# Kernel optimization log

Measured on AMD Instinct MI355X. Metric: run time of the kernel, lower is better.

Reference implementation:

```python
import jax, jax.numpy as jnp
import numpy as np

# nqsystems=8 grouped sites, physical dim d=2^ncontraq=16,
# state bond r=64, layer (unitary MPO) bond rl=16, operator MPO bond ro=4,
# nlsystems=1 pre-contracted circuit layer.
NQ, R, D, RL, RO, NL = 8, 64, 16, 16, 4, 1


def setup_inputs() -> dict:
    key = jax.random.key(0)
    k1, k2, k3 = jax.random.split(key, 3)
    # scale so contractions stay O(1) numerically
    state = jax.random.normal(k1, (NQ, R, D, R), jnp.float32) / np.float32(np.sqrt(R * D))
    layer = jax.random.normal(k2, (NL, NQ, RL, D, D, RL), jnp.float32) / np.float32(np.sqrt(RL * D))
    operator = jax.random.normal(k3, (NQ, RO, D, D, RO), jnp.float32) / np.float32(np.sqrt(RO * D))
    return {"state": state, "layer": layer, "operator": operator}


def reference(state, layer, operator):
    """<psi| U^dagger O U |psi> contracted site-by-site along the TT chain.

    state:    [nq, r, d, r]        TT cores of |psi>
    layer:    [nl, nq, rl, d, d, rl]  TT-operator cores of the circuit layer (nl=1)
    operator: [nq, ro, d, d, ro]   TT-operator cores of the observable
    """
    r, rl, ro = state.shape[1], layer.shape[3], operator.shape[1]
    # open-boundary closure: boundary vectors = e0 on every bond
    env0 = jnp.zeros((r, rl, ro, rl, r), state.dtype).at[0, 0, 0, 0, 0].set(1.0)
    U = layer[0]  # nlsystems == 1

    def step(env, cores):
        S, Uq, Oq = cores
        # tt_dagger: conj + transpose physical indices (0,2,1,3)
        Ud = jnp.conj(Uq).transpose(0, 2, 1, 3)
        # env axes: a=bra-state bond, l=bra-layer bond, o=operator bond,
        #           m=ket-layer bond, b=ket-state bond
        t = jnp.einsum('alomb,aiA->lombiA', env, jnp.conj(S))   # bra state core
        t = jnp.einsum('lombiA,lijL->ombAjL', t, Ud)            # U^dagger core
        t = jnp.einsum('ombAjL,ojkO->mbALkO', t, Oq)            # observable core
        t = jnp.einsum('mbALkO,mksM->bALOsM', t, Uq)            # U core
        t = jnp.einsum('bALOsM,bsB->ALOMB', t, S)               # ket state core
        return t, None

    env, _ = jax.lax.scan(step, env0, (state, U, operator))
    return env[0, 0, 0, 0, 0]
```

## Files before the change

### kernel.cpp

```cpp
#include <hip/hip_runtime.h>


typedef __attribute__((ext_vector_type(8))) short bf16x8;
typedef __attribute__((ext_vector_type(8))) _Float16 f16x8;
typedef __attribute__((ext_vector_type(4))) float f32x4;
typedef __attribute__((ext_vector_type(4))) unsigned short us4;

static __device__ __forceinline__ unsigned short f2bf(float x) {
    union { float f; unsigned u; } a; a.f = x;
    return (unsigned short)((a.u + 0x7FFF + ((a.u >> 16) & 1)) >> 16);
}
static __device__ __forceinline__ float bf2f(unsigned short h) {
    union { unsigned u; float f; } a; a.u = (unsigned)h << 16; return a.f;
}
static __device__ __forceinline__ unsigned split2(float x) {
    unsigned short h = f2bf(x);
    unsigned short l = f2bf(x - bf2f(h));
    return (unsigned)h | ((unsigned)l << 16);
}
static __device__ __forceinline__ void split2_pair(float x0, float x1,
                                                   unsigned& o0, unsigned& o1) {
    unsigned hh, ll;
    asm("v_cvt_pk_bf16_f32 %0, %1, %2" : "=v"(hh) : "v"(x0), "v"(x1));
    union { unsigned u; float f; } c0, c1;
    c0.u = hh << 16;
    c1.u = hh & 0xffff0000u;
    float r0 = x0 - c0.f, r1 = x1 - c1.f;
    asm("v_cvt_pk_bf16_f32 %0, %1, %2" : "=v"(ll) : "v"(r0), "v"(r1));
    asm("v_perm_b32 %0, %1, %2, %3" : "=v"(o0) : "v"(ll), "v"(hh), "s"(0x05040100));
    asm("v_perm_b32 %0, %1, %2, %3" : "=v"(o1) : "v"(ll), "v"(hh), "s"(0x07060302));
}
static __device__ __forceinline__ unsigned short f2h_bits(float x) {
    union { _Float16 h; unsigned short u; } c; c.h = (_Float16)x; return c.u;
}
static __device__ __forceinline__ float h2f_bits(unsigned short u) {
    union { unsigned short u; _Float16 h; } c; c.u = u; return (float)c.h;
}
static __device__ __forceinline__ void gl_lds16(const unsigned short* g,
                                                unsigned short* l) {
    __builtin_amdgcn_global_load_lds(
        (const __attribute__((address_space(1))) unsigned int*)g,
        (__attribute__((address_space(3))) unsigned int*)l, 16, 0, 0);
}

__global__ void write_diag_kernel(float* out, float v) {
    if (threadIdx.x == 0 && blockIdx.x == 0) out[0] = v;
}
__global__ void zero_out(float* o) {
    if (threadIdx.x == 0 && blockIdx.x == 0) o[0] = 0.0f;
}

__global__ void prep_apack(const float* __restrict__ layer,
                           unsigned short* __restrict__ Ap2,
                           unsigned short* __restrict__ Ap4) {
    int idx = blockIdx.x * 256 + threadIdx.x;
    int q = idx >> 13, k0 = (idx >> 10) & 7, mt = (idx >> 6) & 15, lane = idx & 63;
    int quad = lane >> 4, r = lane & 15;
    unsigned short h2[8], l2[8], h4[8], l4[8];
#pragma unroll
    for (int j = 0; j < 8; j++) {
        int k = k0 * 32 + quad * 8 + j;
        int m = mt * 16 + r;
        float v2 = layer[(size_t)q * 65536 +
                         (size_t)((((k >> 4) * 16 + (m >> 4)) * 16 + (k & 15)) * 16 + (m & 15))];
        float v4 = layer[(size_t)q * 65536 +
                         (size_t)((((k >> 4) * 16 + (k & 15)) * 16 + (m >> 4)) * 16 + (m & 15))];
        h2[j] = f2h_bits(v2); l2[j] = f2h_bits(v2 - h2f_bits(h2[j]));
        h4[j] = f2h_bits(v4); l4[j] = f2h_bits(v4 - h2f_bits(h4[j]));
    }
    size_t base = ((size_t)((q * 8 + k0) * 16 + mt) * 2) * 512 + lane * 8;
    *(us4*)(Ap2 + base)       = *(us4*)&h2[0];
    *(us4*)(Ap2 + base + 4)   = *(us4*)&h2[4];
    *(us4*)(Ap2 + base + 512) = *(us4*)&l2[0];
    *(us4*)(Ap2 + base + 516) = *(us4*)&l2[4];
    *(us4*)(Ap4 + base)       = *(us4*)&h4[0];
    *(us4*)(Ap4 + base + 4)   = *(us4*)&h4[4];
    *(us4*)(Ap4 + base + 512) = *(us4*)&l4[0];
    *(us4*)(Ap4 + base + 516) = *(us4*)&l4[4];
}

__global__ void prep_spack1(const float* __restrict__ state,
                            unsigned short* __restrict__ Sp1) {
    int idx = blockIdx.x * 256 + threadIdx.x;
    int q = idx >> 13, c = (idx >> 11) & 3, k0 = (idx >> 10) & 1,
        mt = (idx >> 6) & 15, lane = idx & 63;
    int quad = lane >> 4, lr = lane & 15;
    unsigned short h[8], l[8];
#pragma unroll
    for (int j = 0; j < 8; j++) {
        int k = k0 * 32 + quad * 8 + j;
        float v = state[(size_t)q * 65536 + (size_t)(k * 16 + mt) * 64 + c * 16 + lr];
        h[j] = f2bf(v); l[j] = f2bf(v - bf2f(h[j]));
    }
    size_t base = (size_t)(q * 4 + c) * 32768 + ((size_t)(k0 * 16 + mt) * 2) * 512 + lane * 8;
    *(us4*)(Sp1 + base)       = *(us4*)&h[0];
    *(us4*)(Sp1 + base + 4)   = *(us4*)&h[4];
    *(us4*)(Sp1 + base + 512) = *(us4*)&l[0];
    *(us4*)(Sp1 + base + 516) = *(us4*)&l[4];
}

__global__ void prep_spack5(const float* __restrict__ state,
                            unsigned short* __restrict__ Sp5) {
    int idx = blockIdx.x * 256 + threadIdx.x;
    int q = idx >> 13, k0 = (idx >> 8) & 31, mt = (idx >> 6) & 3, lane = idx & 63;
    int quad = lane >> 4, lr = lane & 15;
    unsigned short h[8], l[8];
#pragma unroll
    for (int j = 0; j < 8; j++) {
        int k = k0 * 32 + quad * 8 + j;
        int s = k >> 6, b = k & 63;
        float v = state[(size_t)q * 65536 + (size_t)(b * 16 + s) * 64 + mt * 16 + lr];
        h[j] = f2bf(v); l[j] = f2bf(v - bf2f(h[j]));
    }
    size_t base = (size_t)q * 131072 + ((size_t)(k0 * 4 + mt) * 2) * 512 + lane * 8;
    *(us4*)(Sp5 + base)       = *(us4*)&h[0];
    *(us4*)(Sp5 + base + 4)   = *(us4*)&h[4];
    *(us4*)(Sp5 + base + 512) = *(us4*)&l[0];
    *(us4*)(Sp5 + base + 516) = *(us4*)&l[4];
}

__global__ void prep_opack3(const float* __restrict__ oper,
                            unsigned short* __restrict__ Op3) {
    int idx = blockIdx.x * 256 + threadIdx.x;
    int q = idx >> 9, k0 = (idx >> 8) & 1, mt = (idx >> 6) & 3, lane = idx & 63;
    int quad = lane >> 4, lr = lane & 15;
    unsigned short h[8], l[8];
#pragma unroll
    for (int j = 0; j < 8; j++) {
        int k = k0 * 32 + quad * 8 + j;
        int m = mt * 16 + lr;
        float v = oper[(size_t)q * 4096 + (size_t)(k * 16 + (m & 15)) * 4 + (m >> 4)];
        h[j] = f2h_bits(v); l[j] = f2h_bits(v - h2f_bits(h[j]));
    }
    size_t base = (size_t)q * 8192 + ((size_t)(k0 * 4 + mt) * 2) * 512 + lane * 8;
    *(us4*)(Op3 + base)       = *(us4*)&h[0];
    *(us4*)(Op3 + base + 4)   = *(us4*)&h[4];
    *(us4*)(Op3 + base + 512) = *(us4*)&l[0];
    *(us4*)(Op3 + base + 516) = *(us4*)&l[4];
}

__global__ void env_split_k(const float* __restrict__ env, unsigned* __restrict__ envS) {
    int t = blockIdx.x * 256 + threadIdx.x;
    float4 v = ((const float4*)env)[t];
    uint4 o;
    o.x = split2(v.x); o.y = split2(v.y); o.z = split2(v.z); o.w = split2(v.w);
    ((uint4*)envS)[t] = o;
}

__global__ void s0_g2(const float* __restrict__ state, const float* __restrict__ layer,
                      float* __restrict__ g2) {
    int t = blockIdx.x * 256 + threadIdx.x;
    int A = t >> 8, j = (t >> 4) & 15, L = t & 15;
    float s = 0;
    for (int i = 0; i < 16; i++) s += state[i * 64 + A] * layer[(j * 16 + i) * 16 + L];
    g2[t] = s;
}
__global__ void s0_g3(const float* __restrict__ g2, const float* __restrict__ oper,
                      float* __restrict__ g3) {
    int t = blockIdx.x * 256 + threadIdx.x;
    int A = t >> 10, L = (t >> 6) & 15, k = (t >> 2) & 15, O = t & 3;
    float s = 0;
    for (int j = 0; j < 16; j++) s += g2[A * 256 + j * 16 + L] * oper[(j * 16 + k) * 4 + O];
    g3[t] = s;
}
__global__ void s0_g4(const float* __restrict__ g3, const float* __restrict__ layer,
                      float* __restrict__ g4) {
    int t = blockIdx.x * 256 + threadIdx.x;
    int A = t >> 14, L = (t >> 10) & 15, O = (t >> 8) & 3, sp = (t >> 4) & 15, M = t & 15;
    float s = 0;
    for (int k = 0; k < 16; k++)
        s += g3[A * 1024 + L * 64 + k * 4 + O] * layer[(k * 16 + sp) * 16 + M];
    g4[t] = s;
}
__global__ void s0_env(const float* __restrict__ g4, const float* __restrict__ state,
                       float* __restrict__ env) {
    int t = blockIdx.x * 256 + threadIdx.x;
    int A = t >> 16, L = (t >> 12) & 15, O = (t >> 10) & 3, M = (t >> 6) & 15, B = t & 63;
    float s = 0;
    for (int sp = 0; sp < 16; sp++)
        s += g4[A * 16384 + L * 1024 + O * 256 + sp * 16 + M] * state[sp * 64 + B];
    env[(size_t)(L * 64 + O * 16 + M) * 4096 + A * 64 + B] = s;
}

__global__ void s7_c1(const float* __restrict__ state, const float* __restrict__ layer,
                      float* __restrict__ c1) {
    int t = blockIdx.x * 256 + threadIdx.x;
    int l = t >> 10, a = (t >> 4) & 63, j = t & 15;
    float s = 0;
    for (int i = 0; i < 16; i++)
        s += state[7 * 65536 + (a * 16 + i) * 64] * layer[7 * 65536 + ((l * 16 + j) * 16 + i) * 16];
    c1[t] = s;
}
__global__ void s7_c2(const float* __restrict__ c1, const float* __restrict__ oper,
                      float* __restrict__ c2) {
    int t = blockIdx.x * 256 + threadIdx.x;
    int o = t >> 14, l = (t >> 10) & 15, a = (t >> 4) & 63, k = t & 15;
    float s = 0;
    for (int j = 0; j < 16; j++)
        s += c1[l * 1024 + a * 16 + j] * oper[7 * 4096 + ((o * 16 + j) * 16 + k) * 4];
    c2[t] = s;
}
__global__ void s7_c3(const float* __restrict__ c2, const float* __restrict__ layer,
                      float* __restrict__ c3) {
    int t = blockIdx.x * 256 + threadIdx.x;
    int m = t >> 16, o = (t >> 14) & 3, l = (t >> 10) & 15, a = (t >> 4) & 63, sp = t & 15;
    float s = 0;
    for (int k = 0; k < 16; k++)
        s += c2[o * 16384 + l * 1024 + a * 16 + k] *
             layer[7 * 65536 + ((m * 16 + k) * 16 + sp) * 16];
    c3[t] = s;
}
__global__ void prep_sv(const float* __restrict__ state, float* __restrict__ sv) {
    int t = blockIdx.x * 256 + threadIdx.x;
    sv[t] = state[7 * 65536 + t * 64];
}
__global__ __launch_bounds__(256) void s7_fused(const float* __restrict__ env,
                                                const float* __restrict__ c3,
                                                const float* __restrict__ sv,
                                                float* __restrict__ out) {
    __shared__ float c3s[1024], svs[1024], red[256];
    int t = threadIdx.x;
    int n0 = blockIdx.x * 64;
    int l = n0 >> 12, o = (n0 >> 10) & 3, m = (n0 >> 6) & 15;
    const float* c3b = c3 + m * 65536 + o * 16384 + l * 1024;
    const float* eb  = env + (size_t)blockIdx.x * 4096;
    for (int i = t; i < 1024; i += 256) { c3s[i] = c3b[i]; svs[i] = sv[i]; }
    __syncthreads();
    float s = 0;
    int b = t & 63, ag = t >> 6;
#pragma unroll
    for (int g = 0; g < 16; g++) {
        int a = ag * 16 + g;
        float e = eb[a * 64 + b];
        float w = 0;
#pragma unroll
        for (int sp = 0; sp < 16; sp++) w += c3s[a * 16 + sp] * svs[b * 16 + sp];
        s += e * w;
    }
    red[t] = s; __syncthreads();
    for (int off = 128; off; off >>= 1) { if (t < off) red[t] += red[t + off]; __syncthreads(); }
    if (t == 0) atomicAdd(out, red[0]);
}

static __device__ __forceinline__ void g1_body(int bid, void* smem,
                                               const unsigned* __restrict__ envS,
                                               const unsigned short* __restrict__ Sp1,
                                               unsigned short* __restrict__ t1,
                                               float scale) {
    unsigned* Bt = (unsigned*)smem;
    const int tid = threadIdx.x, lane = tid & 63, wave = tid >> 6;
    const int quad = lane >> 4, lr = lane & 15;
    const int cc = bid >> 10, rid = bid & 1023;
    const int l = rid >> 6, o = (rid >> 4) & 3, m2 = rid & 15;

    f32x4 acc[4][4];
#pragma unroll
    for (int i = 0; i < 4; i++)
#pragma unroll
        for (int j = 0; j < 4; j++)
#pragma unroll
            for (int r = 0; r < 4; r++) acc[i][j][r] = 0.0f;

    const unsigned* Bv = envS + (size_t)rid * 4096;
    const unsigned short* Sp1c = Sp1 + (size_t)cc * 32768;
    uint4 ur[2];
    auto load_tile = [&](int k0) {
        const uint4* src = (const uint4*)(Bv + k0 * 2048);
        ur[0] = src[tid];
        ur[1] = src[256 + tid];
    };
    auto store_tile = [&]() {
#pragma unroll
        for (int v = 0; v < 2; v++) {
            int e = v * 256 + tid;
            unsigned* p = &Bt[(e >> 4) * 65 + (e & 15) * 4];
            p[0] = ur[v].x; p[1] = ur[v].y; p[2] = ur[v].z; p[3] = ur[v].w;
        }
    };

    bf16x8 ahb[2][4], alb[2][4];
    auto loadA = [&](int k0, int buf) {
#pragma unroll
        for (int mt = 0; mt < 4; mt++) {
            int gmt = wave * 4 + mt;
            const unsigned short* ap = Sp1c + ((size_t)(k0 * 16 + gmt) * 2) * 512 + lane * 8;
            ahb[buf][mt] = *(const bf16x8*)ap;
            alb[buf][mt] = *(const bf16x8*)(ap + 512);
        }
    };

    load_tile(0);
    loadA(0, 0);
    store_tile();
#pragma unroll
    for (int k0 = 0; k0 < 2; k0++) {
        __syncthreads();
        if (k0 + 1 < 2) { load_tile(k0 + 1); loadA(k0 + 1, 1); }
#pragma unroll
        for (int nt = 0; nt < 4; nt++) {
            int nl = nt * 16 + lr;
            bf16x8 bh, bl;
#pragma unroll
            for (int j = 0; j < 8; j++) {
                unsigned u = Bt[(quad * 8 + j) * 65 + nl];
                bh[j] = (short)(u & 0xffffu);
                bl[j] = (short)(u >> 16);
            }
#pragma unroll
            for (int mt = 0; mt < 4; mt++) {
                acc[mt][nt] = __builtin_amdgcn_mfma_f32_16x16x32_bf16(ahb[k0][mt], bh, acc[mt][nt], 0, 0, 0);
                acc[mt][nt] = __builtin_amdgcn_mfma_f32_16x16x32_bf16(ahb[k0][mt], bl, acc[mt][nt], 0, 0, 0);
                acc[mt][nt] = __builtin_amdgcn_mfma_f32_16x16x32_bf16(alb[k0][mt], bh, acc[mt][nt], 0, 0, 0);
            }
        }
        __syncthreads();
        if (k0 + 1 < 2) store_tile();
    }

#pragma unroll
    for (int nt = 0; nt < 4; nt++) {
        int b = nt * 16 + lr;
#pragma unroll
        for (int r = 0; r < 4; r++) {
            int a4 = quad * 4 + r;
            us4 w;
#pragma unroll
            for (int mt = 0; mt < 4; mt++) w[mt] = f2h_bits(acc[mt][nt][r] * scale);
            size_t addr = (size_t)cc * 16777216 +
                          (size_t)(o * 256 + m2 * 16 + a4) * 16384 +
                          (size_t)(l * 2 + (wave >> 1)) * 512 + b * 8 + (wave & 1) * 4;
            *(us4*)(t1 + addr) = w;
        }
    }
}

__global__ __launch_bounds__(256) void gemm_g1(const unsigned* __restrict__ envS,
                                               const unsigned short* __restrict__ Sp1,
                                               unsigned short* __restrict__ t1,
                                               float scale) {
    __shared__ unsigned Bt[32 * 65];
    g1_body(blockIdx.x, Bt, envS, Sp1, t1, scale);
}

static __device__ __forceinline__ void g2_body(int bid, void* smem,
                                               const unsigned short* __restrict__ Bp,
                                               const unsigned short* __restrict__ Ap,
                                               unsigned short* __restrict__ Co) {
    unsigned short* Bs = (unsigned short*)smem;
    const int tid = threadIdx.x, lane = tid & 63, wave = tid >> 6;
    const int quad = lane >> 4, lr = lane & 15;
    const int cc = bid >> 10, rid = bid & 1023;
    const int o = rid >> 8, m2 = (rid >> 4) & 15, a4 = rid & 15;
    const unsigned short* pb = Bp + (size_t)bid * 16384;
    unsigned short* Cb = Co + (size_t)cc * 16777216;

#pragma unroll
    for (int i = 0; i < 8; i++)
        gl_lds16(pb + i * 2048 + tid * 8, Bs + i * 2048 + wave * 512);

    f32x4 acc[4][4];
#pragma unroll
    for (int i = 0; i < 4; i++)
#pragma unroll
        for (int j = 0; j < 4; j++)
#pragma unroll
            for (int r = 0; r < 4; r++) acc[i][j][r] = 0.0f;

    f16x8 ah[3][4];
    auto loadA = [&](int k0, int buf) {
#pragma unroll
        for (int mt = 0; mt < 4; mt++) {
            int gmt = wave * 4 + mt;
            ah[buf][mt] = *(const f16x8*)(Ap + ((size_t)(k0 * 16 + gmt) * 2) * 512 + lane * 8);
        }
    };
    loadA(0, 0);
    loadA(1, 1);

    asm volatile("s_waitcnt vmcnt(0)" ::: "memory");
    __syncthreads();

#pragma unroll
    for (int k0 = 0; k0 < 8; k0++) {
        if (k0 + 2 < 8) loadA(k0 + 2, (k0 + 2) % 3);
        f16x8 bfr[4];
#pragma unroll
        for (int nt = 0; nt < 4; nt++)
            bfr[nt] = *(const f16x8*)(Bs + (k0 * 4 + quad) * 512 + (nt * 16 + lr) * 8);
#pragma unroll
        for (int nt = 0; nt < 4; nt++)
#pragma unroll
            for (int mt = 0; mt < 4; mt++)
                acc[mt][nt] = __builtin_amdgcn_mfma_f32_16x16x32_f16(
                    ah[k0 % 3][mt], bfr[nt], acc[mt][nt], 0, 0, 0);
    }

#pragma unroll
    for (int nt = 0; nt < 4; nt++) {
        int b = nt * 16 + lr;
#pragma unroll
        for (int r = 0; r < 4; r++) {
            int L = quad * 4 + r;
            us4 w;
#pragma unroll
            for (int mt = 0; mt < 4; mt++) w[mt] = f2h_bits(acc[mt][nt][r]);
            size_t addr = (size_t)(L * 256 + m2 * 16 + a4) * 4096 +
                          (size_t)(o * 2 + (wave >> 1)) * 512 + b * 8 + (wave & 1) * 4;
            *(us4*)(Cb + addr) = w;
        }
    }
}

__global__ __launch_bounds__(256) void gemm_g2(const unsigned short* __restrict__ Bp,
                                               const unsigned short* __restrict__ Ap,
                                               unsigned short* __restrict__ Co) {
    __shared__ __align__(16) unsigned short Bs[16384];
    g2_body(blockIdx.x, Bs, Bp, Ap, Co);
}

__global__ __launch_bounds__(256) void fused_g2_g1(
        const unsigned short* __restrict__ Bp,
        const unsigned short* __restrict__ Ap,
        unsigned short* __restrict__ Co,
        const unsigned* __restrict__ envS,
        const unsigned short* __restrict__ Sp1b,
        unsigned short* __restrict__ t1,
        float scale) {
    __shared__ __align__(16) unsigned char smem[32768];
    if (blockIdx.x & 1)
        g1_body(blockIdx.x >> 1, smem, envS, Sp1b, t1, scale);
    else
        g2_body(blockIdx.x >> 1, smem, Bp, Ap, Co);
}

__global__ __launch_bounds__(256) void gemm_g45(const unsigned short* __restrict__ T2,
                                                const unsigned short* __restrict__ Op3q,
                                                const unsigned short* __restrict__ Ap4,
                                                const unsigned short* __restrict__ Sp5,
                                                float* __restrict__ env,
                                                unsigned* __restrict__ envSo,
                                                int A0, float inv, int wf32) {
    __shared__ __align__(16) unsigned short Bs[16384];
    __shared__ unsigned SL[4 * 16 * 68];
    const int tid = threadIdx.x, lane = tid & 63, wave = tid >> 6;
    const int quad = lane >> 4, lr = lane & 15;
    const int cc = blockIdx.x >> 10, rid = blockIdx.x & 1023;
    const int low = rid & 7, O2 = (rid >> 3) & 3, g = rid >> 5;
    const int panel = g * 8 + low;
    const int L = panel >> 4, a4 = panel & 15;
    const unsigned short* T2c = T2 + (size_t)cc * 16777216;
    const int b8 = (wave * 16 + lr) * 8;

    f16x8 ah[3][4];
    auto loadA = [&](int k0, int buf) {
#pragma unroll
        for (int mt = 0; mt < 4; mt++) {
            int gmt = wave * 4 + mt;
            ah[buf][mt] = *(const f16x8*)(Ap4 + ((size_t)(k0 * 16 + gmt) * 2) * 512 + lane * 8);
        }
    };
    loadA(0, 0);
    loadA(1, 1);

    {
        f16x8 oh0 = *(const f16x8*)(Op3q + (size_t)(O2 * 2) * 512 + lane * 8);
        f16x8 oh1 = *(const f16x8*)(Op3q + (size_t)((4 + O2) * 2) * 512 + lane * 8);
        f16x8 tb[5][2];
        auto loadT2 = [&](int m2, int buf) {
            const unsigned short* pp = T2c + (size_t)(L * 256 + m2 * 16 + a4) * 4096;
            tb[buf][0] = *(const f16x8*)(pp + (quad << 9) + b8);
            tb[buf][1] = *(const f16x8*)(pp + ((4 + quad) << 9) + b8);
        };
        loadT2(0, 0); loadT2(1, 1); loadT2(2, 2); loadT2(3, 3);
#pragma unroll
        for (int m2 = 0; m2 < 16; m2++) {
            if (m2 + 4 < 16) loadT2(m2 + 4, (m2 + 4) % 5);
            f32x4 a3;
            a3[0] = a3[1] = a3[2] = a3[3] = 0.0f;
            a3 = __builtin_amdgcn_mfma_f32_16x16x32_f16(oh0, tb[m2 % 5][0], a3, 0, 0, 0);
            a3 = __builtin_amdgcn_mfma_f32_16x16x32_f16(oh1, tb[m2 % 5][1], a3, 0, 0, 0);
            us4 w;
#pragma unroll
            for (int r = 0; r < 4; r++) w[r] = f2h_bits(a3[r]);
            *(us4*)(Bs + (m2 * 2 + (quad >> 1)) * 512 + b8 + (quad & 1) * 4) = w;
        }
    }
    __syncthreads();

    f32x4 acc[4][4];
#pragma unroll
    for (int i = 0; i < 4; i++)
#pragma unroll
        for (int j = 0; j < 4; j++)
#pragma unroll
            for (int r = 0; r < 4; r++) acc[i][j][r] = 0.0f;

#pragma unroll
    for (int k0 = 0; k0 < 8; k0++) {
        if (k0 + 2 < 8) loadA(k0 + 2, (k0 + 2) % 3);
        f16x8 bfr[4];
#pragma unroll
        for (int nt = 0; nt < 4; nt++)
            bfr[nt] = *(const f16x8*)(Bs + (k0 * 4 + quad) * 512 + (nt * 16 + lr) * 8);
#pragma unroll
        for (int nt = 0; nt < 4; nt++)
#pragma unroll
            for (int mt = 0; mt < 4; mt++)
                acc[mt][nt] = __builtin_amdgcn_mfma_f32_16x16x32_f16(
                    ah[k0 % 3][mt], bfr[nt], acc[mt][nt], 0, 0, 0);
    }

    unsigned* myslab = SL + wave * (16 * 68);
    f32x4 acc5[4];
#pragma unroll
    for (int nt = 0; nt < 4; nt++)
#pragma unroll
        for (int r = 0; r < 4; r++) acc5[nt][r] = 0.0f;

    bf16x8 s5h[2][4], s5l[2][4];
    auto loadS5 = [&](int step, int buf) {
        int kg = (wave * 4 + (step >> 1)) * 2 + (step & 1);
#pragma unroll
        for (int nt = 0; nt < 4; nt++) {
            const unsigned short* bp = Sp5 + ((size_t)(kg * 4 + nt) * 2) * 512 + lane * 8;
            s5h[buf][nt] = *(const bf16x8*)bp;
            s5l[buf][nt] = *(const bf16x8*)(bp + 512);
        }
    };
    loadS5(0, 0);

#pragma unroll
    for (int mtp = 0; mtp < 4; mtp++) {
#pragma unroll
        for (int nt = 0; nt < 4; nt++) {
            unsigned o0, o1, o2, o3;
            split2_pair(acc[mtp][nt][0], acc[mtp][nt][1], o0, o1);
            split2_pair(acc[mtp][nt][2], acc[mtp][nt][3], o2, o3);
            myslab[(quad * 4 + 0) * 68 + nt * 16 + lr] = o0;
            myslab[(quad * 4 + 1) * 68 + nt * 16 + lr] = o1;
            myslab[(quad * 4 + 2) * 68 + nt * 16 + lr] = o2;
            myslab[(quad * 4 + 3) * 68 + nt * 16 + lr] = o3;
        }
        asm volatile("s_waitcnt lgkmcnt(0)" ::: "memory");
#pragma unroll
        for (int h = 0; h < 2; h++) {
            const int step = mtp * 2 + h;
            const unsigned* sp = &myslab[lr * 68 + h * 32 + quad * 8];
            uint4 u0 = *(const uint4*)sp;
            uint4 u1 = *(const uint4*)(sp + 4);
            bf16x8 th, tl;
            th[0] = (short)(u0.x & 0xffff); tl[0] = (short)(u0.x >> 16);
            th[1] = (short)(u0.y & 0xffff); tl[1] = (short)(u0.y >> 16);
            th[2] = (short)(u0.z & 0xffff); tl[2] = (short)(u0.z >> 16);
            th[3] = (short)(u0.w & 0xffff); tl[3] = (short)(u0.w >> 16);
            th[4] = (short)(u1.x & 0xffff); tl[4] = (short)(u1.x >> 16);
            th[5] = (short)(u1.y & 0xffff); tl[5] = (short)(u1.y >> 16);
            th[6] = (short)(u1.z & 0xffff); tl[6] = (short)(u1.z >> 16);
            th[7] = (short)(u1.w & 0xffff); tl[7] = (short)(u1.w >> 16);
            if (step + 1 < 8) loadS5(step + 1, (step + 1) & 1);
#pragma unroll
            for (int nt = 0; nt < 4; nt++) {
                acc5[nt] = __builtin_amdgcn_mfma_f32_16x16x32_bf16(th, s5h[step & 1][nt], acc5[nt], 0, 0, 0);
                acc5[nt] = __builtin_amdgcn_mfma_f32_16x16x32_bf16(th, s5l[step & 1][nt], acc5[nt], 0, 0, 0);
                acc5[nt] = __builtin_amdgcn_mfma_f32_16x16x32_bf16(tl, s5h[step & 1][nt], acc5[nt], 0, 0, 0);
            }
        }
    }

    __syncthreads();
    float* red = (float*)SL;
#pragma unroll
    for (int nt = 0; nt < 4; nt++)
#pragma unroll
        for (int r = 0; r < 4; r++)
            red[wave * 1088 + (quad * 4 + r) * 68 + nt * 16 + lr] = acc5[nt][r];
    __syncthreads();
    float wv[4];
#pragma unroll
    for (int r = 0; r < 4; r++) {
        int M2 = quad * 4 + r, Bc = wave * 16 + lr;
        float v = red[M2 * 68 + Bc] + red[1088 + M2 * 68 + Bc] +
                  red[2176 + M2 * 68 + Bc] + red[3264 + M2 * 68 + Bc];
        wv[r] = v * inv;
    }
    unsigned s0p, s1p, s2p, s3p;
    split2_pair(wv[0], wv[1], s0p, s1p);
    split2_pair(wv[2], wv[3], s2p, s3p);
    unsigned sp4[4] = {s0p, s1p, s2p, s3p};
#pragma unroll
    for (int r = 0; r < 4; r++) {
        int M2 = quad * 4 + r, Bc = wave * 16 + lr;
        size_t idx = (size_t)(L * 64 + O2 * 16 + M2) * 4096 + (A0 + cc * 16 + a4) * 64 + Bc;
        envSo[idx] = sp4[r];
        if (wf32) env[idx] = wv[r];
    }
}

extern "C" void kernel_launch(void* const* d_in, const int* in_sizes, int n_in,
                              void* d_out, int out_size, void* d_ws, size_t ws_size,
                              hipStream_t stream) {
    const float* state = (const float*)d_in[0];
    const float* layer = (const float*)d_in[1];
    const float* oper  = (const float*)d_in[2];
    float* out = (float*)d_out;

    const size_t need = 16777216ull * 4 + 33554432ull * 4 + 3ull * 4194304ull * 4 +
                        (4ull * 1048576ull + 65536ull) * 2ull + 4096ull;
    if (ws_size < need) {
        write_diag_kernel<<<1, 64, 0, stream>>>(out, (float)ws_size);
        return;
    }
    float* F    = (float*)d_ws;
    unsigned* P = (unsigned*)(F + 16777216);
    unsigned* envS0 = (unsigned*)(P + 33554432);
    float* envB = (float*)(envS0 + 4194304);
    unsigned* envS1 = (unsigned*)(envB + 4194304);
    unsigned short* Ap2 = (unsigned short*)(envS1 + 4194304);
    unsigned short* Ap4 = Ap2 + 1048576;
    unsigned short* Sp1 = Ap4 + 1048576;
    unsigned short* Sp5 = Sp1 + 1048576;
    unsigned short* Op3 = Sp5 + 1048576;
    float* sv = (float*)(Op3 + 65536);
    float* SCR = F;
    unsigned short* T1p0 = (unsigned short*)P;
    unsigned short* T1p1 = T1p0 + 33554432;
    unsigned short* T2 = (unsigned short*)F;

    prep_apack<<<256, 256, 0, stream>>>(layer, Ap2, Ap4);
    prep_spack1<<<256, 256, 0, stream>>>(state, Sp1);
    prep_spack5<<<256, 256, 0, stream>>>(state, Sp5);
    prep_opack3<<<16, 256, 0, stream>>>(oper, Op3);
    prep_sv<<<4, 256, 0, stream>>>(state, sv);

    s0_g2<<<64, 256, 0, stream>>>(state, layer, SCR);
    s0_g3<<<256, 256, 0, stream>>>(SCR, oper, SCR + 16384);
    s0_g4<<<4096, 256, 0, stream>>>(SCR + 16384, layer, SCR + 81920);
    s0_env<<<16384, 256, 0, stream>>>(SCR + 81920, state, envB);
    env_split_k<<<4096, 256, 0, stream>>>(envB, envS1);

    for (int q = 1; q < 7; q++) {
        unsigned* einS  = (q & 1) ? envS1 : envS0;
        unsigned* eoutS = (q & 1) ? envS0 : envS1;
        float scl = (float)(1u << (16 + 2 * q));
        float inv = 1.0f / scl;
        int wf32 = (q == 6) ? 1 : 0;
        gemm_g1<<<2048, 256, 0, stream>>>(
            einS, Sp1 + (size_t)(q * 4 + 0) * 32768, T1p0, scl);
        fused_g2_g1<<<4096, 256, 0, stream>>>(
            T1p0, Ap2 + (size_t)q * 131072, T2,
            einS, Sp1 + (size_t)(q * 4 + 2) * 32768, T1p1, scl);
        gemm_g45<<<2048, 256, 0, stream>>>(
            T2, Op3 + (size_t)q * 8192, Ap4 + (size_t)q * 131072,
            Sp5 + (size_t)q * 131072, envB, eoutS, 0, inv, wf32);
        gemm_g2<<<2048, 256, 0, stream>>>(
            T1p1, Ap2 + (size_t)q * 131072, T2);
        gemm_g45<<<2048, 256, 0, stream>>>(
            T2, Op3 + (size_t)q * 8192, Ap4 + (size_t)q * 131072,
            Sp5 + (size_t)q * 131072, envB, eoutS, 32, inv, wf32);
    }

    s7_c1<<<64, 256, 0, stream>>>(state, layer, SCR);
    s7_c2<<<256, 256, 0, stream>>>(SCR, oper, SCR + 16384);
    s7_c3<<<4096, 256, 0, stream>>>(SCR + 16384, layer, SCR + 81920);
    zero_out<<<1, 64, 0, stream>>>(out);
    s7_fused<<<1024, 256, 0, stream>>>(envB, SCR + 81920, sv, out);
}
```

Baseline: 1.381 ms.

## Fuse g45 of first half with g2 of second half in one launch

Merges the first g45 contraction and the second-half g2 GEMM into a single interleaved kernel, double-buffering T2 by reusing the T1p0 buffer, which is dead by then. Blocks now alternate between the two bodies in groups of eight rather than one by one, and the same grouping is applied to the existing g2/g1 fusion. The goal is to cut a launch and its tail bubble per iteration and let compute-heavy and memory-heavy work share the GPU. The fused kernel reserves the larger g45 shared-memory footprint for every block, which may lower occupancy for the g2 blocks.

```diff
diff --git a/kernel.cpp b/kernel.cpp
--- a/kernel.cpp
+++ b/kernel.cpp
@@ -411,40 +411,19 @@
     }
 }
 
-__global__ __launch_bounds__(256) void gemm_g2(const unsigned short* __restrict__ Bp,
-                                               const unsigned short* __restrict__ Ap,
-                                               unsigned short* __restrict__ Co) {
-    __shared__ __align__(16) unsigned short Bs[16384];
-    g2_body(blockIdx.x, Bs, Bp, Ap, Co);
-}
-
-__global__ __launch_bounds__(256) void fused_g2_g1(
-        const unsigned short* __restrict__ Bp,
-        const unsigned short* __restrict__ Ap,
-        unsigned short* __restrict__ Co,
-        const unsigned* __restrict__ envS,
-        const unsigned short* __restrict__ Sp1b,
-        unsigned short* __restrict__ t1,
-        float scale) {
-    __shared__ __align__(16) unsigned char smem[32768];
-    if (blockIdx.x & 1)
-        g1_body(blockIdx.x >> 1, smem, envS, Sp1b, t1, scale);
-    else
-        g2_body(blockIdx.x >> 1, smem, Bp, Ap, Co);
-}
-
-__global__ __launch_bounds__(256) void gemm_g45(const unsigned short* __restrict__ T2,
+static __device__ __forceinline__ void g45_body(int bid, void* smem,
+                                                const unsigned short* __restrict__ T2,
                                                 const unsigned short* __restrict__ Op3q,
                                                 const unsigned short* __restrict__ Ap4,
                                                 const unsigned short* __restrict__ Sp5,
                                                 float* __restrict__ env,
                                                 unsigned* __restrict__ envSo,
                                                 int A0, float inv, int wf32) {
-    __shared__ __align__(16) unsigned short Bs[16384];
-    __shared__ unsigned SL[4 * 16 * 68];
+    unsigned short* Bs = (unsigned short*)smem;
+    unsigned* SL = (unsigned*)((char*)smem + 32768);
     const int tid = threadIdx.x, lane = tid & 63, wave = tid >> 6;
     const int quad = lane >> 4, lr = lane & 15;
-    const int cc = blockIdx.x >> 10, rid = blockIdx.x & 1023;
+    const int cc = bid >> 10, rid = bid & 1023;
     const int low = rid & 7, O2 = (rid >> 3) & 3, g = rid >> 5;
     const int panel = g * 8 + low;
     const int L = panel >> 4, a4 = panel & 15;
@@ -596,6 +575,53 @@
     }
 }
 
+__global__ __launch_bounds__(256) void gemm_g45(const unsigned short* __restrict__ T2,
+                                                const unsigned short* __restrict__ Op3q,
+                                                const unsigned short* __restrict__ Ap4,
+                                                const unsigned short* __restrict__ Sp5,
+                                                float* __restrict__ env,
+                                                unsigned* __restrict__ envSo,
+                                                int A0, float inv, int wf32) {
+    __shared__ __align__(16) unsigned char smem[50176];
+    g45_body(blockIdx.x, smem, T2, Op3q, Ap4, Sp5, env, envSo, A0, inv, wf32);
+}
+
+__global__ __launch_bounds__(256) void fused_g2_g1(
+        const unsigned short* __restrict__ Bp,
+        const unsigned short* __restrict__ Ap,
+        unsigned short* __restrict__ Co,
+        const unsigned* __restrict__ envS,
+        const unsigned short* __restrict__ Sp1b,
+        unsigned short* __restrict__ t1,
+        float scale) {
+    __shared__ __align__(16) unsigned char smem[32768];
+    const int grp = blockIdx.x >> 3;
+    const int sub = (grp >> 1) * 8 + (blockIdx.x & 7);
+    if (grp & 1)
+        g1_body(sub, smem, envS, Sp1b, t1, scale);
+    else
+        g2_body(sub, smem, Bp, Ap, Co);
+}
+
+__global__ __launch_bounds__(256) void fused_g45_g2(
+        const unsigned short* __restrict__ T2a,
+        const unsigned short* __restrict__ Op3q,
+        const unsigned short* __restrict__ Ap4,
+        const unsigned short* __restrict__ Sp5,
+        float* __restrict__ env, unsigned* __restrict__ envSo,
+        float inv, int wf32,
+        const unsigned short* __restrict__ Bp,
+        const unsigned short* __restrict__ Ap,
+        unsigned short* __restrict__ Co) {
+    __shared__ __align__(16) unsigned char smem[50176];
+    const int grp = blockIdx.x >> 3;
+    const int sub = (grp >> 1) * 8 + (blockIdx.x & 7);
+    if (grp & 1)
+        g2_body(sub, smem, Bp, Ap, Co);
+    else
+        g45_body(sub, smem, T2a, Op3q, Ap4, Sp5, env, envSo, 0, inv, wf32);
+}
+
 extern "C" void kernel_launch(void* const* d_in, const int* in_sizes, int n_in,
                               void* d_out, int out_size, void* d_ws, size_t ws_size,
                               hipStream_t stream) {
@@ -624,7 +650,8 @@
     float* SCR = F;
     unsigned short* T1p0 = (unsigned short*)P;
     unsigned short* T1p1 = T1p0 + 33554432;
-    unsigned short* T2 = (unsigned short*)F;
+    unsigned short* T2p0 = (unsigned short*)F;
+    unsigned short* T2p1 = T1p0;
 
     prep_apack<<<256, 256, 0, stream>>>(layer, Ap2, Ap4);
     prep_spack1<<<256, 256, 0, stream>>>(state, Sp1);
@@ -647,15 +674,14 @@
         gemm_g1<<<2048, 256, 0, stream>>>(
             einS, Sp1 + (size_t)(q * 4 + 0) * 32768, T1p0, scl);
         fused_g2_g1<<<4096, 256, 0, stream>>>(
-            T1p0, Ap2 + (size_t)q * 131072, T2,
+            T1p0, Ap2 + (size_t)q * 131072, T2p0,
             einS, Sp1 + (size_t)(q * 4 + 2) * 32768, T1p1, scl);
+        fused_g45_g2<<<4096, 256, 0, stream>>>(
+            T2p0, Op3 + (size_t)q * 8192, Ap4 + (size_t)q * 131072,
+            Sp5 + (size_t)q * 131072, envB, eoutS, inv, wf32,
+            T1p1, Ap2 + (size_t)q * 131072, T2p1);
         gemm_g45<<<2048, 256, 0, stream>>>(
-            T2, Op3 + (size_t)q * 8192, Ap4 + (size_t)q * 131072,
-            Sp5 + (size_t)q * 131072, envB, eoutS, 0, inv, wf32);
-        gemm_g2<<<2048, 256, 0, stream>>>(
-            T1p1, Ap2 + (size_t)q * 131072, T2);
-        gemm_g45<<<2048, 256, 0, stream>>>(
-            T2, Op3 + (size_t)q * 8192, Ap4 + (size_t)q * 131072,
+            T2p1, Op3 + (size_t)q * 8192, Ap4 + (size_t)q * 131072,
             Sp5 + (size_t)q * 131072, envB, eoutS, 32, inv, wf32);
     }
 
```

Result: faster. 1.301 ms (-5.8%).
